# Optimization experiments

Measured on AMD Instinct MI355X. Metric: run time of the kernel, lower is better.

The kernel has to match this reference:

```python
import jax, jax.numpy as jnp
import numpy as np
from jax import lax

B, S, D, H = 2, 2048, 1024, 16
DEPTH = D // H  # 64


def _leaky(x):
    # tf.keras.layers.ReLU(negative_slope=0.1)
    return jnp.where(x >= 0, x, 0.1 * x)


def _split_heads(x):
    # [B,S,D] -> [B,H,S,DEPTH]
    return x.reshape(B, S, H, DEPTH).transpose(0, 2, 1, 3)


def setup_inputs() -> dict:
    key = jax.random.key(0)
    ks = jax.random.split(key, 8)
    w = lambda k: 0.02 * jax.random.normal(k, (D, D), dtype=jnp.float32)
    return {
        "q": jax.random.normal(ks[0], (B, S, D), dtype=jnp.float32),
        "k": jax.random.normal(ks[1], (B, S, D), dtype=jnp.float32),
        "v": jax.random.normal(ks[2], (B, S, D), dtype=jnp.float32),
        "query_mask": jnp.ones((B, S, 1), dtype=jnp.float32),
        "key_mask": jnp.ones((B, S, 1), dtype=jnp.float32),
        "value_mask": jnp.ones((B, S, 1), dtype=jnp.float32),
        "Wq": w(ks[3]), "bq": 0.5 * jnp.ones((D,), dtype=jnp.float32),
        "Wk": w(ks[4]), "bk": 0.5 * jnp.ones((D,), dtype=jnp.float32),
        "Wv": w(ks[5]), "bv": jnp.zeros((D,), dtype=jnp.float32),
        "Wo": w(ks[6]), "bo": jnp.zeros((D,), dtype=jnp.float32),
    }


def _causal_linear_attn(qh, kh, vh):
    # qh,kh,vh: [B,H,S,DEPTH]. Sequential recurrence:
    #   S_t = S_{t-1} + k_t v_t^T ; z_t = z_{t-1} + k_t
    #   out_t = (q_t @ S_t) / (q_t . z_t)
    def step(carry, x):
        S_st, z = carry
        qi, ki, vi = x  # each [B,H,DEPTH]
        S_st = S_st + ki[..., :, None] * vi[..., None, :]  # [B,H,DEPTH,DEPTH]
        z = z + ki
        num = jnp.einsum('bhd,bhde->bhe', qi, S_st)
        den = jnp.einsum('bhd,bhd->bh', qi, z)
        return (S_st, z), num / den[..., None]

    init = (jnp.zeros((B, H, DEPTH, DEPTH), dtype=qh.dtype),
            jnp.zeros((B, H, DEPTH), dtype=qh.dtype))
    xs = (jnp.moveaxis(qh, 2, 0), jnp.moveaxis(kh, 2, 0), jnp.moveaxis(vh, 2, 0))
    _, out = lax.scan(step, init, xs)  # [S,B,H,DEPTH]
    return jnp.moveaxis(out, 0, 2)  # [B,H,S,DEPTH]


def reference(q, k, v, query_mask, key_mask, value_mask,
              Wq, bq, Wk, bk, Wv, bv, Wo, bo):
    q = (q * query_mask) @ Wq + bq
    k = (k * key_mask) @ Wk + bk
    v = (v * value_mask) @ Wv + bv
    q = _leaky(q)
    k = _leaky(k)
    qh, kh, vh = _split_heads(q), _split_heads(k), _split_heads(v)
    attn = _causal_linear_attn(qh, kh, vh)  # [B,H,S,DEPTH]
    concat = attn.transpose(0, 2, 1, 3).reshape(B, S, D)
    return concat @ Wo + bo
```

## Files before the change

### kernel.cpp

```cpp
#include <hip/hip_runtime.h>

#define Bx    2
#define Sx    2048
#define Dx    1024
#define Hx    16
#define NCx   (Sx/64)
#define BHx   (Bx*Hx)
#define Mx    (Bx*Sx)

typedef float    f4 __attribute__((ext_vector_type(4)));
typedef _Float16 h8 __attribute__((ext_vector_type(8)));
typedef _Float16 h4 __attribute__((ext_vector_type(4)));

__device__ __forceinline__ void gl2lds16(const _Float16* g, _Float16* l) {
  __builtin_amdgcn_global_load_lds(
      (const __attribute__((address_space(1))) void*)g,
      (__attribute__((address_space(3))) void*)l, 16, 0, 0);
}

__global__ __launch_bounds__(256) void convert_w(
    const float* __restrict__ W0, const float* __restrict__ W1,
    const float* __restrict__ W2, const float* __restrict__ W3,
    _Float16* __restrict__ T0, _Float16* __restrict__ T1,
    _Float16* __restrict__ T2, _Float16* __restrict__ T3)
{
  const float* W = (blockIdx.z == 0) ? W0 : (blockIdx.z == 1) ? W1 :
                   (blockIdx.z == 2) ? W2 : W3;
  _Float16* T = (blockIdx.z == 0) ? T0 : (blockIdx.z == 1) ? T1 :
                (blockIdx.z == 2) ? T2 : T3;
  __shared__ float Ws[64 * 68];
  const int tx = threadIdx.x & 15, ty = threadIdx.x >> 4;
  const int k0 = blockIdx.y * 64, n0 = blockIdx.x * 64;
#pragma unroll
  for (int i = 0; i < 4; i++) {
    const int r = ty + 16 * i;
    *(f4*)&Ws[r * 68 + tx * 4] = *(const f4*)&W[(size_t)(k0 + r) * Dx + n0 + tx * 4];
  }
  __syncthreads();
#pragma unroll
  for (int i = 0; i < 4; i++) {
    const int n = ty + 16 * i;
    h4 o;
#pragma unroll
    for (int j = 0; j < 4; j++) o[j] = (_Float16)Ws[(tx * 4 + j) * 68 + n];
    *(h4*)&T[(size_t)(n0 + n) * Dx + k0 + tx * 4] = o;
  }
}

struct GArgs {
  const void* A; const _Float16* Bt; const float* bias; const float* mask;
  void* out; int leaky, half_out;
};

template<int BN, int WR, int WC, int A32>
__global__ __launch_bounds__(512, 4) void gemm_f16(GArgs g0, GArgs g1, GArgs g2)
{
  const GArgs g = (blockIdx.z == 0) ? g0 : (blockIdx.z == 1) ? g1 : g2;
  constexpr int FM = 128 / WR / 16;
  constexpr int FN = BN / WC / 16;
  __shared__ _Float16 As[128 * 64];
  __shared__ _Float16 Bs[BN * 64];
  const int tid = threadIdx.x;
  const int m0 = blockIdx.y * 128, n0 = blockIdx.x * BN;
  const int lane = tid & 63, wave = tid >> 6;
  const int lm = lane & 15, qd = lane >> 4;
  const int wr = wave % WR, wc = wave / WR;
  const int wm0 = wr * (128 / WR), wn0 = wc * (BN / WC);
  const int srow = lane >> 3;
  const int sseg = (lane & 7) ^ srow;
  const _Float16* gB = g.Bt + (size_t)(n0 + srow) * Dx + sseg * 8;

  const _Float16* gA16 = nullptr;
  const float* gA32[2];
  float mf[2];
  if (A32) {
#pragma unroll
    for (int u = 0; u < 2; u++) {
      const int r = m0 + (wave * 2 + u) * 8 + srow;
      gA32[u] = (const float*)g.A + (size_t)r * Dx + sseg * 8;
      mf[u] = g.mask[r];
    }
  } else {
    gA16 = (const _Float16*)g.A + (size_t)(m0 + srow) * Dx + sseg * 8;
  }

  f4 acc[FM][FN];
#pragma unroll
  for (int i = 0; i < FM; i++)
#pragma unroll
    for (int j = 0; j < FN; j++) { f4 z = {0.f, 0.f, 0.f, 0.f}; acc[i][j] = z; }

  for (int kt = 0; kt < Dx; kt += 64) {
    __syncthreads();
    if (A32) {
#pragma unroll
      for (int u = 0; u < 2; u++) {
        const f4 a0 = *(const f4*)(gA32[u] + kt);
        const f4 a1 = *(const f4*)(gA32[u] + kt + 4);
        h8 o;
#pragma unroll
        for (int i = 0; i < 4; i++) {
          o[i]     = (_Float16)(a0[i] * mf[u]);
          o[4 + i] = (_Float16)(a1[i] * mf[u]);
        }
        *(h8*)&As[(wave * 2 + u) * 512 + lane * 8] = o;
      }
    } else {
#pragma unroll
      for (int u = 0; u < 2; u++) {
        const int t = wave * 2 + u;
        gl2lds16(gA16 + (size_t)(t * 8) * Dx + kt, &As[t * 512]);
      }
    }
#pragma unroll
    for (int u = 0; u < BN / 64; u++) {
      const int t = wave * (BN / 64) + u;
      gl2lds16(gB + (size_t)(t * 8) * Dx + kt, &Bs[t * 512]);
    }
    __syncthreads();
#pragma unroll
    for (int kk = 0; kk < 2; kk++) {
      const int sp = ((kk * 4 + qd) ^ (lm & 7)) * 8;
      h8 af[FM];
#pragma unroll
      for (int i = 0; i < FM; i++)
        af[i] = *(const h8*)&As[(wm0 + i * 16 + lm) * 64 + sp];
#pragma unroll
      for (int j = 0; j < FN; j++) {
        const h8 bf = *(const h8*)&Bs[(wn0 + j * 16 + lm) * 64 + sp];
#pragma unroll
        for (int i = 0; i < FM; i++)
          acc[i][j] = __builtin_amdgcn_mfma_f32_16x16x32_f16(af[i], bf, acc[i][j], 0, 0, 0);
      }
    }
  }

#pragma unroll
  for (int j = 0; j < FN; j++) {
    const int n = n0 + wn0 + j * 16 + lm;
    const float bz = g.bias[n];
#pragma unroll
    for (int i = 0; i < FM; i++) {
      const int mb = m0 + wm0 + i * 16 + qd * 4;
#pragma unroll
      for (int r = 0; r < 4; r++) {
        float v = acc[i][j][r] + bz;
        if (g.leaky) v = (v >= 0.f) ? v : 0.1f * v;
        if (g.half_out) ((_Float16*)g.out)[(size_t)(mb + r) * Dx + n] = (_Float16)v;
        else            ((float*)g.out)[(size_t)(mb + r) * Dx + n] = v;
      }
    }
  }
}

__global__ __launch_bounds__(256) void chunkkv_mfma(
    const _Float16* __restrict__ kp, const _Float16* __restrict__ vp,
    _Float16* __restrict__ ckvh, float* __restrict__ cz)
{
  __shared__ _Float16 Kt[64 * 64];
  __shared__ _Float16 Vt[64 * 64];
  const int blk = blockIdx.x;
  const int c = blk & (NCx - 1);
  const int bh = blk / NCx;
  const int b = bh / Hx, h = bh % Hx;
  const int tid = threadIdx.x;
  const size_t rowbase = ((size_t)(b * Sx + c * 64)) * Dx + h * 64;

#pragma unroll
  for (int p = 0; p < 2; p++) {
    const int f = tid + 256 * p;
    const int s = f >> 3, g8 = f & 7;
    const h8 hk = *(const h8*)&kp[rowbase + (size_t)s * Dx + g8 * 8];
    const h8 hv = *(const h8*)&vp[rowbase + (size_t)s * Dx + g8 * 8];
#pragma unroll
    for (int i = 0; i < 8; i++) {
      const int r = g8 * 8 + i;
      const int a = r * 64 + (((s >> 3) ^ (r & 7)) * 8) + (s & 7);
      Kt[a] = hk[i];
      Vt[a] = hv[i];
    }
  }
  __syncthreads();

  const int lane = tid & 63, w = tid >> 6;
  const int lm = lane & 15, qd = lane >> 4;
  const int x7 = lm & 7;

  h8 av[2];
#pragma unroll
  for (int kk = 0; kk < 2; kk++)
    av[kk] = *(const h8*)&Vt[(w * 16 + lm) * 64 + (((kk << 2) + qd) ^ x7) * 8];

#pragma unroll
  for (int dt = 0; dt < 4; dt++) {
    f4 acc = {0.f, 0.f, 0.f, 0.f};
#pragma unroll
    for (int kk = 0; kk < 2; kk++) {
      const h8 bf = *(const h8*)&Kt[(dt * 16 + lm) * 64 + (((kk << 2) + qd) ^ x7) * 8];
      acc = __builtin_amdgcn_mfma_f32_16x16x32_f16(av[kk], bf, acc, 0, 0, 0);
    }
#pragma unroll
    for (int r = 0; r < 4; r++) {
      const int e = w * 16 + qd * 4 + r;
      ckvh[(size_t)blk * 4096 + e * 64 + dt * 16 + lm] = (_Float16)acc[r];
    }
  }

  {
    const int d = tid >> 2, fr = tid & 3;
    float dp = 0.f;
#pragma unroll
    for (int j = 0; j < 2; j++) {
      const h8 kv = *(const h8*)&Kt[d * 64 + (fr * 2 + j) * 8];
#pragma unroll
      for (int i = 0; i < 8; i++) dp += (float)kv[i];
    }
    dp += __shfl_xor(dp, 1);
    dp += __shfl_xor(dp, 2);
    if (fr == 0) cz[(size_t)blk * 64 + d] = dp;
  }
}

__global__ __launch_bounds__(256) void prefix_kernel(
    _Float16* __restrict__ ckvh, float* __restrict__ cz)
{
  const int gid = blockIdx.x * 256 + threadIdx.x;
  const int bh = gid >> 12, el = gid & 4095;
  const size_t base = (((size_t)bh * NCx) << 12) + el;
  float vals[NCx];
#pragma unroll
  for (int c = 0; c < NCx; c++)
    vals[c] = (float)ckvh[base + ((size_t)c << 12)];
  float acc = 0.f;
#pragma unroll
  for (int c = 0; c < NCx; c++) { const float t = vals[c]; vals[c] = acc; acc += t; }
#pragma unroll
  for (int c = 0; c < NCx; c++)
    ckvh[base + ((size_t)c << 12)] = (_Float16)vals[c];

  if (gid < BHx * 64) {
    const int zbh = gid >> 6, d = gid & 63;
    const size_t zb = (size_t)zbh * NCx * 64 + d;
    float zv[NCx];
#pragma unroll
    for (int c = 0; c < NCx; c++) zv[c] = cz[zb + (size_t)c * 64];
    float az = 0.f;
#pragma unroll
    for (int c = 0; c < NCx; c++) { const float t = zv[c]; zv[c] = az; az += t; }
#pragma unroll
    for (int c = 0; c < NCx; c++) cz[zb + (size_t)c * 64] = zv[c];
  }
}

__global__ __launch_bounds__(256) void attn_mfma(
    const _Float16* __restrict__ qp, const _Float16* __restrict__ kp,
    const _Float16* __restrict__ vp, const _Float16* __restrict__ ckvh,
    const float* __restrict__ cz, _Float16* __restrict__ concat)
{
  __shared__ _Float16 Qs[64 * 64];
  __shared__ _Float16 Ks[64 * 64];
  __shared__ _Float16 Vt[64 * 64];
  __shared__ _Float16 Sh[64 * 64];
  __shared__ float zs[64];
  __shared__ float den[64];
  const int blk = blockIdx.x;
  const int c = blk & (NCx - 1);
  const int bh = blk / NCx;
  const int b = bh / Hx, h = bh % Hx;
  const int tid = threadIdx.x;
  const size_t rowbase = ((size_t)(b * Sx + c * 64)) * Dx + h * 64;

#pragma unroll
  for (int p = 0; p < 2; p++) {
    const int f = tid + 256 * p;
    const int r = f >> 3, sg = f & 7;
    const int ph = (sg ^ (r & 7)) * 8;
    *(h8*)&Qs[r * 64 + ph] = *(const h8*)&qp[rowbase + (size_t)r * Dx + sg * 8];
    *(h8*)&Ks[r * 64 + ph] = *(const h8*)&kp[rowbase + (size_t)r * Dx + sg * 8];
    *(h8*)&Sh[r * 64 + ph] = *(const h8*)&ckvh[(size_t)blk * 4096 + r * 64 + sg * 8];
  }
#pragma unroll
  for (int p = 0; p < 2; p++) {
    const int f = tid + 256 * p;
    const int s = f >> 3, g8 = f & 7;
    const h8 hv = *(const h8*)&vp[rowbase + (size_t)s * Dx + g8 * 8];
#pragma unroll
    for (int i = 0; i < 8; i++) {
      const int e = g8 * 8 + i;
      Vt[e * 64 + (((s >> 3) ^ (e & 7)) * 8) + (s & 7)] = hv[i];
    }
  }
  if (tid < 64) zs[tid] = cz[(size_t)blk * 64 + tid];
  __syncthreads();

  const int lane = tid & 63, w = tid >> 6;
  const int lm = lane & 15, qd = lane >> 4;
  const int x7 = lm & 7;

  h8 aq[2];
#pragma unroll
  for (int kk = 0; kk < 2; kk++)
    aq[kk] = *(const h8*)&Qs[(w * 16 + lm) * 64 + (((kk << 2) + qd) ^ x7) * 8];

  f4 pc[4];
#pragma unroll
  for (int st = 0; st < 4; st++) {
    f4 z4 = {0.f, 0.f, 0.f, 0.f}; pc[st] = z4;
#pragma unroll
    for (int kk = 0; kk < 2; kk++) {
      const h8 bf = *(const h8*)&Ks[(st * 16 + lm) * 64 + (((kk << 2) + qd) ^ x7) * 8];
      pc[st] = __builtin_amdgcn_mfma_f32_16x16x32_f16(aq[kk], bf, pc[st], 0, 0, 0);
    }
  }
  float rsum[4] = {0.f, 0.f, 0.f, 0.f};
#pragma unroll
  for (int st = 0; st < 4; st++) {
    const int s = st * 16 + lm;
#pragma unroll
    for (int r = 0; r < 4; r++) {
      const int t = w * 16 + qd * 4 + r;
      float v = pc[st][r];
      v = (s <= t) ? v : 0.f;
      pc[st][r] = v;
      rsum[r] += v;
    }
  }
#pragma unroll
  for (int r = 0; r < 4; r++) {
    rsum[r] += __shfl_xor(rsum[r], 1);
    rsum[r] += __shfl_xor(rsum[r], 2);
    rsum[r] += __shfl_xor(rsum[r], 4);
    rsum[r] += __shfl_xor(rsum[r], 8);
  }
  {
    const int t = tid >> 2, fr = tid & 3;
    float dp = 0.f;
#pragma unroll
    for (int j = 0; j < 2; j++) {
      const int sg = fr * 2 + j;
      const h8 qv = *(const h8*)&Qs[t * 64 + (sg ^ (t & 7)) * 8];
#pragma unroll
      for (int i = 0; i < 8; i++) dp += (float)qv[i] * zs[sg * 8 + i];
    }
    dp += __shfl_xor(dp, 1);
    dp += __shfl_xor(dp, 2);
    if (fr == 0) den[t] = dp;
  }
  __syncthreads();

  _Float16* Pa = Ks;
#pragma unroll
  for (int st = 0; st < 4; st++) {
#pragma unroll
    for (int r = 0; r < 4; r++) {
      const int row = w * 16 + qd * 4 + r;
      Pa[row * 64 + (((st * 2 + (lm >> 3)) ^ (row & 7)) * 8) + (lm & 7)] =
          (_Float16)pc[st][r];
    }
  }
  if (lm == 0) {
#pragma unroll
    for (int r = 0; r < 4; r++) den[w * 16 + qd * 4 + r] += rsum[r];
  }
  __syncthreads();

  h8 ap[2];
#pragma unroll
  for (int kk = 0; kk < 2; kk++)
    ap[kk] = *(const h8*)&Pa[(w * 16 + lm) * 64 + (((kk << 2) + qd) ^ x7) * 8];

  f4 acc[4];
#pragma unroll
  for (int et = 0; et < 4; et++) {
    f4 z4 = {0.f, 0.f, 0.f, 0.f}; acc[et] = z4;
#pragma unroll
    for (int kk = 0; kk < 2; kk++) {
      const h8 bv = *(const h8*)&Vt[(et * 16 + lm) * 64 + (((kk << 2) + qd) ^ x7) * 8];
      acc[et] = __builtin_amdgcn_mfma_f32_16x16x32_f16(ap[kk], bv, acc[et], 0, 0, 0);
    }
#pragma unroll
    for (int kk = 0; kk < 2; kk++) {
      const h8 bs = *(const h8*)&Sh[(et * 16 + lm) * 64 + (((kk << 2) + qd) ^ x7) * 8];
      acc[et] = __builtin_amdgcn_mfma_f32_16x16x32_f16(aq[kk], bs, acc[et], 0, 0, 0);
    }
  }

#pragma unroll
  for (int r = 0; r < 4; r++) {
    const int row = w * 16 + qd * 4 + r;
    const float inv = 1.f / den[row];
    _Float16* orow = &concat[((size_t)(b * Sx + c * 64 + row)) * Dx + h * 64];
#pragma unroll
    for (int et = 0; et < 4; et++)
      orow[et * 16 + lm] = (_Float16)(acc[et][r] * inv);
  }
}

extern "C" void kernel_launch(void* const* d_in, const int* in_sizes, int n_in,
                              void* d_out, int out_size, void* d_ws, size_t ws_size,
                              hipStream_t stream)
{
  const float* q  = (const float*)d_in[0];
  const float* k  = (const float*)d_in[1];
  const float* v  = (const float*)d_in[2];
  const float* qm = (const float*)d_in[3];
  const float* km = (const float*)d_in[4];
  const float* vm = (const float*)d_in[5];
  const float* Wq = (const float*)d_in[6];
  const float* bq = (const float*)d_in[7];
  const float* Wk = (const float*)d_in[8];
  const float* bk = (const float*)d_in[9];
  const float* Wv = (const float*)d_in[10];
  const float* bv = (const float*)d_in[11];
  const float* Wo = (const float*)d_in[12];
  const float* bo = (const float*)d_in[13];
  float* out = (float*)d_out;

  char* ws = (char*)d_ws;
  _Float16* ckvh   = (_Float16*)(ws);
  _Float16* concat = (_Float16*)(ws + 8388608);
  _Float16* Wtq = (_Float16*)(ws + 25165824);
  _Float16* Wtk = (_Float16*)(ws + 27262976);
  _Float16* Wtv = (_Float16*)(ws + 29360128);
  _Float16* Wto = (_Float16*)(ws + 31457280);
  _Float16* qp  = (_Float16*)(ws + 33554432);
  _Float16* kp  = (_Float16*)(ws + 41943040);
  _Float16* vp  = (_Float16*)(ws + 50331648);
  float*    cz  = (float*)   (ws + 58720256);

  convert_w<<<dim3(16, 16, 4), 256, 0, stream>>>(Wq, Wk, Wv, Wo, Wtq, Wtk, Wtv, Wto);

  GArgs gq = { q, Wtq, bq, qm, qp, 1, 1 };
  GArgs gk = { k, Wtk, bk, km, kp, 1, 1 };
  GArgs gv = { v, Wtv, bv, vm, vp, 0, 1 };
  gemm_f16<128, 4, 2, 1><<<dim3(Dx / 128, Mx / 128, 3), 512, 0, stream>>>(gq, gk, gv);

  chunkkv_mfma<<<BHx * NCx, 256, 0, stream>>>(kp, vp, ckvh, cz);
  prefix_kernel<<<512, 256, 0, stream>>>(ckvh, cz);
  attn_mfma<<<BHx * NCx, 256, 0, stream>>>(qp, kp, vp, ckvh, cz, concat);

  GArgs go = { concat, Wto, bo, nullptr, out, 0, 0 };
  gemm_f16<64, 4, 2, 0><<<dim3(Dx / 64, Mx / 128, 1), 512, 0, stream>>>(go, go, go);
}
```

Baseline: 212.8 us.

## Remap GEMM workgroups across XCDs, prefetch fp32 A, reswizzle transposed LDS tiles

The GEMM remaps the linear workgroup index so that consecutive tiles are spread round-robin over the eight XCDs, aiming to improve L2 locality for shared A and B tiles. It also software-prefetches the next fp32 A slice into registers before the barrier, so global load latency overlaps with the MFMA work. The transposed K/V LDS layouts in the chunk and output kernels gain an extra XOR term on the row's upper bits, intended to cut bank conflicts on the scattered transpose stores. The prefetch adds register pressure, and the remap hardcodes a grid height of 32.

```diff
diff --git a/kernel.cpp b/kernel.cpp
--- a/kernel.cpp
+++ b/kernel.cpp
@@ -55,13 +55,22 @@
 template<int BN, int WR, int WC, int A32>
 __global__ __launch_bounds__(512, 4) void gemm_f16(GArgs g0, GArgs g1, GArgs g2)
 {
-  const GArgs g = (blockIdx.z == 0) ? g0 : (blockIdx.z == 1) ? g1 : g2;
+  constexpr int GX  = Dx / BN;
+  constexpr int LGX = (GX == 8) ? 3 : 4;
+  const int wgp = blockIdx.x + GX * (blockIdx.y + 32 * blockIdx.z);
+  const int nwg = GX * 32 * gridDim.z;
+  const int wgl = (wgp & 7) * (nwg >> 3) + (wgp >> 3);
+  const int bxx = wgl & (GX - 1);
+  const int byy = (wgl >> LGX) & 31;
+  const int bzz = wgl >> (LGX + 5);
+
+  const GArgs g = (bzz == 0) ? g0 : (bzz == 1) ? g1 : g2;
   constexpr int FM = 128 / WR / 16;
   constexpr int FN = BN / WC / 16;
   __shared__ _Float16 As[128 * 64];
   __shared__ _Float16 Bs[BN * 64];
   const int tid = threadIdx.x;
-  const int m0 = blockIdx.y * 128, n0 = blockIdx.x * BN;
+  const int m0 = byy * 128, n0 = bxx * BN;
   const int lane = tid & 63, wave = tid >> 6;
   const int lm = lane & 15, qd = lane >> 4;
   const int wr = wave % WR, wc = wave / WR;
@@ -73,12 +82,15 @@
   const _Float16* gA16 = nullptr;
   const float* gA32[2];
   float mf[2];
+  f4 pa0[2], pa1[2];
   if (A32) {
 #pragma unroll
     for (int u = 0; u < 2; u++) {
       const int r = m0 + (wave * 2 + u) * 8 + srow;
       gA32[u] = (const float*)g.A + (size_t)r * Dx + sseg * 8;
       mf[u] = g.mask[r];
+      pa0[u] = *(const f4*)(gA32[u]);
+      pa1[u] = *(const f4*)(gA32[u] + 4);
     }
   } else {
     gA16 = (const _Float16*)g.A + (size_t)(m0 + srow) * Dx + sseg * 8;
@@ -95,13 +107,11 @@
     if (A32) {
 #pragma unroll
       for (int u = 0; u < 2; u++) {
-        const f4 a0 = *(const f4*)(gA32[u] + kt);
-        const f4 a1 = *(const f4*)(gA32[u] + kt + 4);
         h8 o;
 #pragma unroll
         for (int i = 0; i < 4; i++) {
-          o[i]     = (_Float16)(a0[i] * mf[u]);
-          o[4 + i] = (_Float16)(a1[i] * mf[u]);
+          o[i]     = (_Float16)(pa0[u][i] * mf[u]);
+          o[4 + i] = (_Float16)(pa1[u][i] * mf[u]);
         }
         *(h8*)&As[(wave * 2 + u) * 512 + lane * 8] = o;
       }
@@ -116,6 +126,13 @@
     for (int u = 0; u < BN / 64; u++) {
       const int t = wave * (BN / 64) + u;
       gl2lds16(gB + (size_t)(t * 8) * Dx + kt, &Bs[t * 512]);
+    }
+    if (A32 && kt + 64 < Dx) {
+#pragma unroll
+      for (int u = 0; u < 2; u++) {
+        pa0[u] = *(const f4*)(gA32[u] + kt + 64);
+        pa1[u] = *(const f4*)(gA32[u] + kt + 68);
+      }
     }
     __syncthreads();
 #pragma unroll
@@ -175,7 +192,7 @@
 #pragma unroll
     for (int i = 0; i < 8; i++) {
       const int r = g8 * 8 + i;
-      const int a = r * 64 + (((s >> 3) ^ (r & 7)) * 8) + (s & 7);
+      const int a = r * 64 + ((((s >> 3) ^ (r & 7)) ^ ((r >> 3) & 7)) * 8) + (s & 7);
       Kt[a] = hk[i];
       Vt[a] = hv[i];
     }
@@ -184,19 +201,24 @@
 
   const int lane = tid & 63, w = tid >> 6;
   const int lm = lane & 15, qd = lane >> 4;
-  const int x7 = lm & 7;
 
   h8 av[2];
-#pragma unroll
-  for (int kk = 0; kk < 2; kk++)
-    av[kk] = *(const h8*)&Vt[(w * 16 + lm) * 64 + (((kk << 2) + qd) ^ x7) * 8];
+  {
+    const int rv = w * 16 + lm;
+    const int xv = (rv & 7) ^ ((rv >> 3) & 7);
+#pragma unroll
+    for (int kk = 0; kk < 2; kk++)
+      av[kk] = *(const h8*)&Vt[rv * 64 + ((((kk << 2) + qd)) ^ xv) * 8];
+  }
 
 #pragma unroll
   for (int dt = 0; dt < 4; dt++) {
+    const int rk = dt * 16 + lm;
+    const int xk = (rk & 7) ^ ((rk >> 3) & 7);
     f4 acc = {0.f, 0.f, 0.f, 0.f};
 #pragma unroll
     for (int kk = 0; kk < 2; kk++) {
-      const h8 bf = *(const h8*)&Kt[(dt * 16 + lm) * 64 + (((kk << 2) + qd) ^ x7) * 8];
+      const h8 bf = *(const h8*)&Kt[rk * 64 + ((((kk << 2) + qd)) ^ xk) * 8];
       acc = __builtin_amdgcn_mfma_f32_16x16x32_f16(av[kk], bf, acc, 0, 0, 0);
     }
 #pragma unroll
@@ -208,10 +230,11 @@
 
   {
     const int d = tid >> 2, fr = tid & 3;
+    const int dx = (d & 7) ^ ((d >> 3) & 7);
     float dp = 0.f;
 #pragma unroll
     for (int j = 0; j < 2; j++) {
-      const h8 kv = *(const h8*)&Kt[d * 64 + (fr * 2 + j) * 8];
+      const h8 kv = *(const h8*)&Kt[d * 64 + ((fr * 2 + j) ^ dx) * 8];
 #pragma unroll
       for (int i = 0; i < 8; i++) dp += (float)kv[i];
     }
@@ -287,7 +310,7 @@
 #pragma unroll
     for (int i = 0; i < 8; i++) {
       const int e = g8 * 8 + i;
-      Vt[e * 64 + (((s >> 3) ^ (e & 7)) * 8) + (s & 7)] = hv[i];
+      Vt[e * 64 + ((((s >> 3) ^ (e & 7)) ^ ((e >> 3) & 7)) * 8) + (s & 7)] = hv[i];
     }
   }
   if (tid < 64) zs[tid] = cz[(size_t)blk * 64 + tid];
@@ -372,15 +395,17 @@
   f4 acc[4];
 #pragma unroll
   for (int et = 0; et < 4; et++) {
+    const int re = et * 16 + lm;
+    const int xv = (re & 7) ^ ((re >> 3) & 7);
     f4 z4 = {0.f, 0.f, 0.f, 0.f}; acc[et] = z4;
 #pragma unroll
     for (int kk = 0; kk < 2; kk++) {
-      const h8 bv = *(const h8*)&Vt[(et * 16 + lm) * 64 + (((kk << 2) + qd) ^ x7) * 8];
+      const h8 bv = *(const h8*)&Vt[re * 64 + ((((kk << 2) + qd)) ^ xv) * 8];
       acc[et] = __builtin_amdgcn_mfma_f32_16x16x32_f16(ap[kk], bv, acc[et], 0, 0, 0);
     }
 #pragma unroll
     for (int kk = 0; kk < 2; kk++) {
-      const h8 bs = *(const h8*)&Sh[(et * 16 + lm) * 64 + (((kk << 2) + qd) ^ x7) * 8];
+      const h8 bs = *(const h8*)&Sh[re * 64 + (((kk << 2) + qd) ^ x7) * 8];
       acc[et] = __builtin_amdgcn_mfma_f32_16x16x32_f16(aq[kk], bs, acc[et], 0, 0, 0);
     }
   }
```

New measurement: 209.3 us. About the same (-1.6%).
